# Kernel tuning notes

Measured on AMD Instinct MI355X. Metric: run time of the kernel, lower is better.

The kernel has to match this reference:

```python
import jax, jax.numpy as jnp
import numpy as np

N_NEURONS, D_MODEL, D_FF, N_PATTERNS, K_PATTERNS = 2048, 1024, 4096, 64, 4
B, S, K = 4, 2048, 8


def setup_inputs() -> dict:
    key = jax.random.key(0)
    ks = jax.random.split(key, 10)
    return {
        "x": jax.random.normal(ks[0], (B, S, D_MODEL), jnp.float32),
        "router_out": jax.random.normal(ks[1], (B, S, D_MODEL), jnp.float32),
        "topk_neuron_idx": jax.random.randint(ks[2], (B, S, K), 0, N_NEURONS),
        "topk_neuron_weights": jax.random.uniform(ks[3], (B, S, K), jnp.float32),
        "selected_neurons": jax.random.normal(ks[4], (B, S, K, D_MODEL), jnp.float32),
        "pattern_queries": jax.random.normal(ks[5], (N_PATTERNS, D_MODEL), jnp.float32) * 0.02,
        "gates": jax.random.normal(ks[6], (N_PATTERNS, D_FF), jnp.float32) * 0.02,
        "up_w": jax.random.normal(ks[7], (D_FF, D_MODEL), jnp.float32) / np.sqrt(D_MODEL),
        "up_b": jnp.zeros((D_FF,), jnp.float32),
        "down_w": jax.random.normal(ks[8], (D_MODEL, D_FF), jnp.float32) / np.sqrt(D_FF),
        "down_b": jnp.zeros((D_MODEL,), jnp.float32),
    }


def reference(x, router_out, topk_neuron_idx, topk_neuron_weights, selected_neurons,
              pattern_queries, gates, up_w, up_b, down_w, down_b):
    D = selected_neurons.shape[-1]
    # pattern scoring: [P, B, S, K]
    sim = jnp.einsum('pd,bskd->pbsk', pattern_queries, selected_neurons) / jnp.sqrt(jnp.float32(D))
    pattern_scores = jnp.einsum('pbsk,bsk->bsp', sim, topk_neuron_weights)  # weighted sum over K, permuted
    topk_scores, topk_pattern_idx = jax.lax.top_k(pattern_scores, K_PATTERNS)  # [B,S,k]
    topk_pattern_weights = jax.nn.softmax(topk_scores, axis=-1)
    selected_gates = gates[topk_pattern_idx]  # [B,S,k,d_ff]
    ffn_gate = jnp.einsum('bsk,bskf->bsf', topk_pattern_weights, selected_gates)
    h = jnp.einsum('bsd,fd->bsf', x, up_w) + up_b
    h = jax.nn.gelu(h * jax.nn.sigmoid(ffn_gate), approximate=False)
    return jnp.einsum('bsf,df->bsd', h, down_w) + down_b
```

## Files before the change

### kernel.cpp

```cpp
#include <hip/hip_runtime.h>
#include <hip/hip_bf16.h>
#include <math.h>

#define R_   8192
#define DM   1024
#define DFF  4096
#define NP   64
#define KN   8

typedef __bf16 bf16x8 __attribute__((ext_vector_type(8)));
typedef float  f32x4  __attribute__((ext_vector_type(4)));

__device__ __forceinline__ unsigned short f2bf(float f) {
  union { float f; unsigned u; } v; v.f = f;
  unsigned u = v.u;
  return (unsigned short)((u + 0x7FFFu + ((u >> 16) & 1u)) >> 16);
}

__device__ __forceinline__ float dot4(const float4 a, const float4 b) {
  return a.x * b.x + a.y * b.y + a.z * b.z + a.w * b.w;
}

__device__ __forceinline__ void fma4(float4& a, float w, const float4 s) {
  a.x += w * s.x; a.y += w * s.y; a.z += w * s.z; a.w += w * s.w;
}

__global__ __launch_bounds__(256) void cvt_bf16_kernel(
    const float* __restrict__ in, unsigned short* __restrict__ out, int n8) {
  int i = blockIdx.x * 256 + threadIdx.x;
  if (i >= n8) return;
  const float4* p = (const float4*)in + (size_t)i * 2;
  float4 a = p[0], b = p[1];
  uint4 r;
  r.x = (unsigned)f2bf(a.x) | ((unsigned)f2bf(a.y) << 16);
  r.y = (unsigned)f2bf(a.z) | ((unsigned)f2bf(a.w) << 16);
  r.z = (unsigned)f2bf(b.x) | ((unsigned)f2bf(b.y) << 16);
  r.w = (unsigned)f2bf(b.z) | ((unsigned)f2bf(b.w) << 16);
  ((uint4*)out)[i] = r;
}

__global__ __launch_bounds__(256) void vcomp_kernel(
    const float* __restrict__ sn,
    const float* __restrict__ tw,
    float* __restrict__ v)
{
  const int r = blockIdx.x;
  const int t = threadIdx.x;
  float w[KN];
#pragma unroll
  for (int k = 0; k < KN; ++k) w[k] = tw[(size_t)r * KN + k];
  const float* base = sn + (size_t)r * (KN * DM) + t * 4;
  float4 a = {0.f, 0.f, 0.f, 0.f};
#pragma unroll
  for (int k = 0; k < KN; ++k) fma4(a, w[k], *(const float4*)(base + k * DM));
  *(float4*)(v + (size_t)r * DM + t * 4) = a;
}

__global__ __launch_bounds__(256, 2) void score_kernel(
    const float* __restrict__ v,
    const float* __restrict__ pq,
    int*   __restrict__ out_idx,
    float* __restrict__ out_w)
{
  const int lane = threadIdx.x & 63;
  const int wave = threadIdx.x >> 6;
  const int pos0 = (blockIdx.x * 4 + wave) * 4;

  float4 vr[4][4];
#pragma unroll
  for (int p = 0; p < 4; ++p) {
    const float4* s = (const float4*)(v + (size_t)(pos0 + p) * DM + lane * 16);
    vr[p][0] = s[0]; vr[p][1] = s[1]; vr[p][2] = s[2]; vr[p][3] = s[3];
  }

  float sreg[4];
#pragma unroll 1
  for (int pat = 0; pat < NP; ++pat) {
    const float4* q = (const float4*)(pq + pat * DM + lane * 16);
    const float4 q0 = q[0], q1 = q[1], q2 = q[2], q3 = q[3];
    float part[4];
#pragma unroll
    for (int p = 0; p < 4; ++p)
      part[p] = dot4(q0, vr[p][0]) + dot4(q1, vr[p][1]) +
                dot4(q2, vr[p][2]) + dot4(q3, vr[p][3]);
#pragma unroll
    for (int off = 32; off >= 1; off >>= 1) {
#pragma unroll
      for (int p = 0; p < 4; ++p)
        part[p] += __shfl_xor(part[p], off, 64);
    }
    if (lane == pat) {
#pragma unroll
      for (int p = 0; p < 4; ++p) sreg[p] = part[p] * 0.03125f;
    }
  }

#pragma unroll
  for (int p = 0; p < 4; ++p) {
    float cur = sreg[p];
    float m0, m1, m2, m3; int i0, i1, i2, i3;
#define ARGMAX_STEP(MV, MI)                                   \
    {                                                         \
      float bv = cur; int bi = lane;                          \
      _Pragma("unroll")                                       \
      for (int off = 32; off >= 1; off >>= 1) {               \
        float ov = __shfl_xor(bv, off, 64);                   \
        int   oi = __shfl_xor(bi, off, 64);                   \
        if (ov > bv || (ov == bv && oi < bi)) { bv = ov; bi = oi; } \
      }                                                       \
      MV = bv; MI = bi;                                       \
      if (lane == bi) cur = -3.0e38f;                         \
    }
    ARGMAX_STEP(m0, i0) ARGMAX_STEP(m1, i1) ARGMAX_STEP(m2, i2) ARGMAX_STEP(m3, i3)
#undef ARGMAX_STEP
    const float e1 = __expf(m1 - m0), e2 = __expf(m2 - m0), e3 = __expf(m3 - m0);
    const float inv = 1.f / (1.f + e1 + e2 + e3);
    if (lane < 4) {
      const int r = pos0 + p;
      const int myi = (lane == 0) ? i0 : (lane == 1) ? i1 : (lane == 2) ? i2 : i3;
      const float mye = (lane == 0) ? 1.f : (lane == 1) ? e1 : (lane == 2) ? e2 : e3;
      out_idx[r * 4 + lane] = myi;
      out_w[r * 4 + lane] = mye * inv;
    }
  }
}

__device__ __forceinline__ void gll16(const void* g, void* l) {
  __builtin_amdgcn_global_load_lds(
      (const __attribute__((address_space(1))) unsigned int*)g,
      (__attribute__((address_space(3))) unsigned int*)l, 16, 0, 0);
}


#define LGKM0 asm volatile("s_waitcnt lgkmcnt(0)" ::: "memory")
#define VMC(N) asm volatile("s_waitcnt vmcnt(%0)" ::"i"(N) : "memory")

__global__ __launch_bounds__(256, 2) void gemm1_kernel(
    const unsigned short* __restrict__ A,
    const unsigned short* __restrict__ Bm,
    const float* __restrict__ bias,
    const int*   __restrict__ pidx,
    const float* __restrict__ pwt,
    const float* __restrict__ gates,
    unsigned short* __restrict__ H)
{
  extern __shared__ char smem[];
  constexpr int K_ = 1024, NT = 32;
  const int tid = threadIdx.x, lane = tid & 63, wid = tid >> 6;
  const int wr = wid >> 1, wc = wid & 1;
  const int cpx = gridDim.x >> 3;
  const int swzb = ((int)blockIdx.x & 7) * cpx + ((int)blockIdx.x >> 3);
  const int brow = swzb >> 5, bcol = swzb & 31;

  const unsigned short* Ab = A  + (size_t)brow * 256 * K_;
  const unsigned short* Bb = Bm + (size_t)bcol * 128 * K_;

  const int aSrc = (wid * 16 + (lane >> 2)) * K_ +
                   (((lane & 3) ^ ((lane >> 2) & 3)) * 8);
  const int ldsSt = wid * 1024;
  const int laneRd = (lane & 15) * 64 + (((lane >> 4) ^ (lane & 3)) * 16);
  const int aRd = wr * 8192 + laneRd;
  const int bRd = 16384 + wc * 4096 + laneRd;

  f32x4 acc[8][4];
#pragma unroll
  for (int m = 0; m < 8; ++m)
#pragma unroll
    for (int n = 0; n < 4; ++n) acc[m][n] = (f32x4){0.f, 0.f, 0.f, 0.f};

#define G1_STA(BO, PG) { _Pragma("unroll") for (int i_ = 0; i_ < 4; ++i_)     \
    gll16((PG) + i_ * 64 * K_ + aSrc, smem + (BO) + i_ * 4096 + ldsSt); }
#define G1_STB(BO, PG) { _Pragma("unroll") for (int i_ = 0; i_ < 2; ++i_)     \
    gll16((PG) + i_ * 64 * K_ + aSrc, smem + (BO) + 16384 + i_ * 4096 + ldsSt); }

  G1_STA(0, Ab)           G1_STB(0, Bb)
  G1_STA(24576, Ab + 32)  G1_STB(24576, Bb + 32)
  G1_STB(49152, Bb + 64)
  VMC(8);
  __builtin_amdgcn_s_barrier();

  int o0 = 0, o1 = 24576, o2 = 49152;
#pragma unroll 1
  for (int j = 0; j < NT; ++j) {
    bf16x8 a[4], b[4];
    {
      const char* pa = smem + o0 + aRd;
      const char* pb = smem + o0 + bRd;
#pragma unroll
      for (int m = 0; m < 4; ++m) a[m] = *(const bf16x8*)(pa + m * 1024);
#pragma unroll
      for (int n = 0; n < 4; ++n) b[n] = *(const bf16x8*)(pb + n * 1024);
    }
    if (j < NT - 2) G1_STA(o2, Ab + (j + 2) * 32)
    LGKM0;
    __builtin_amdgcn_s_barrier();
    __builtin_amdgcn_s_setprio(1);
#pragma unroll
    for (int m = 0; m < 4; ++m)
#pragma unroll
      for (int n = 0; n < 4; ++n)
        acc[m][n] = __builtin_amdgcn_mfma_f32_16x16x32_bf16(a[m], b[n], acc[m][n], 0, 0, 0);
    __builtin_amdgcn_s_setprio(0);
    {
      const char* pa = smem + o0 + aRd + 4096;
#pragma unroll
      for (int m = 0; m < 4; ++m) a[m] = *(const bf16x8*)(pa + m * 1024);
    }
    if (j < NT - 3) G1_STB(o0, Bb + (j + 3) * 32)
    LGKM0;
    if (j < NT - 2) { VMC(6); } else { VMC(0); }
    __builtin_amdgcn_s_barrier();
    __builtin_amdgcn_s_setprio(1);
#pragma unroll
    for (int m = 0; m < 4; ++m)
#pragma unroll
      for (int n = 0; n < 4; ++n)
        acc[4 + m][n] = __builtin_amdgcn_mfma_f32_16x16x32_bf16(a[m], b[n], acc[4 + m][n], 0, 0, 0);
    __builtin_amdgcn_s_setprio(0);
    const int t = o0; o0 = o1; o1 = o2; o2 = t;
  }
#undef G1_STA
#undef G1_STB

  const int crow0 = brow * 256 + wr * 128;
  const int ccol0 = bcol * 128 + wc * 64 + (lane & 15);
  const int rsub  = (lane >> 4) * 4;
#pragma unroll
  for (int m = 0; m < 8; ++m) {
    const int rbase = crow0 + m * 16 + rsub;
    int   ia[4][4];
    float wa[4][4];
#pragma unroll
    for (int j = 0; j < 4; ++j) {
      const int4   iq = *(const int4*)(pidx + (size_t)(rbase + j) * 4);
      const float4 wq = *(const float4*)(pwt + (size_t)(rbase + j) * 4);
      ia[j][0] = iq.x; ia[j][1] = iq.y; ia[j][2] = iq.z; ia[j][3] = iq.w;
      wa[j][0] = wq.x; wa[j][1] = wq.y; wa[j][2] = wq.z; wa[j][3] = wq.w;
    }
#pragma unroll
    for (int n = 0; n < 4; ++n) {
      const int col = ccol0 + n * 16;
      const float ub = bias[col];
#pragma unroll
      for (int j = 0; j < 4; ++j) {
        float g = wa[j][0] * gates[(size_t)ia[j][0] * DFF + col]
                + wa[j][1] * gates[(size_t)ia[j][1] * DFF + col]
                + wa[j][2] * gates[(size_t)ia[j][2] * DFF + col]
                + wa[j][3] * gates[(size_t)ia[j][3] * DFF + col];
        const float u   = acc[m][n][j] + ub;
        const float val = u * (1.f / (1.f + __expf(-g)));
        const float h   = 0.5f * val * (1.f + erff(val * 0.70710678118654752f));
        H[(size_t)(rbase + j) * DFF + col] = f2bf(h);
      }
    }
  }
}

__global__ __launch_bounds__(256, 2) void gemm2_kernel(
    const unsigned short* __restrict__ A,
    const unsigned short* __restrict__ Bm,
    const float* __restrict__ bias,
    float* __restrict__ O)
{
  extern __shared__ char smem[];
  constexpr int K_ = 4096, NT = 128;
  const int tid = threadIdx.x, lane = tid & 63, wid = tid >> 6;
  const int wr = wid >> 1, wc = wid & 1;
  const int cpx = gridDim.x >> 3;
  const int swzb = ((int)blockIdx.x & 7) * cpx + ((int)blockIdx.x >> 3);
  const int brow = swzb >> 3, bcol = swzb & 7;

  const unsigned short* Ab = A  + (size_t)brow * 128 * K_;
  const unsigned short* Bb = Bm + (size_t)bcol * 128 * K_;

  const int aSrc = (wid * 16 + (lane >> 2)) * K_ +
                   (((lane & 3) ^ ((lane >> 2) & 3)) * 8);
  const int ldsSt = wid * 1024;
  const int laneRd = (lane & 15) * 64 + (((lane >> 4) ^ (lane & 3)) * 16);
  const int aRd = wr * 4096 + laneRd;
  const int bRd = 8192 + wc * 4096 + laneRd;

  f32x4 acc[4][4];
#pragma unroll
  for (int m = 0; m < 4; ++m)
#pragma unroll
    for (int n = 0; n < 4; ++n) acc[m][n] = (f32x4){0.f, 0.f, 0.f, 0.f};

#define G2_ST(BO, PGA, PGB) {                                                 \
    _Pragma("unroll") for (int i_ = 0; i_ < 2; ++i_)                          \
      gll16((PGA) + i_ * 64 * K_ + aSrc, smem + (BO) + i_ * 4096 + ldsSt);    \
    _Pragma("unroll") for (int i_ = 0; i_ < 2; ++i_)                          \
      gll16((PGB) + i_ * 64 * K_ + aSrc, smem + (BO) + 8192 + i_ * 4096 + ldsSt); }

  G2_ST(0,     Ab,      Bb)
  G2_ST(16384, Ab + 32, Bb + 32)
  G2_ST(32768, Ab + 64, Bb + 64)
  VMC(8);
  __builtin_amdgcn_s_barrier();

  int o0 = 0, o1 = 16384, o2 = 32768, o3 = 49152;
#pragma unroll 1
  for (int j = 0; j < NT; ++j) {
    bf16x8 a[4], b[4];
    {
      const char* pa = smem + o0 + aRd;
      const char* pb = smem + o0 + bRd;
#pragma unroll
      for (int m = 0; m < 4; ++m) a[m] = *(const bf16x8*)(pa + m * 1024);
#pragma unroll
      for (int n = 0; n < 4; ++n) b[n] = *(const bf16x8*)(pb + n * 1024);
    }
    if (j < NT - 3) G2_ST(o3, Ab + (j + 3) * 32, Bb + (j + 3) * 32)
    LGKM0;
    if (j < NT - 3)      { VMC(8); }
    else if (j == NT - 3){ VMC(4); }
    else                 { VMC(0); }
    __builtin_amdgcn_s_barrier();
    __builtin_amdgcn_s_setprio(1);
#pragma unroll
    for (int m = 0; m < 4; ++m)
#pragma unroll
      for (int n = 0; n < 4; ++n)
        acc[m][n] = __builtin_amdgcn_mfma_f32_16x16x32_bf16(a[m], b[n], acc[m][n], 0, 0, 0);
    __builtin_amdgcn_s_setprio(0);
    const int t = o0; o0 = o1; o1 = o2; o2 = o3; o3 = t;
  }
#undef G2_ST

  const int crow0 = brow * 128 + wr * 64;
  const int ccol0 = bcol * 128 + wc * 64 + (lane & 15);
  const int rsub  = (lane >> 4) * 4;
#pragma unroll
  for (int m = 0; m < 4; ++m) {
    const int rbase = crow0 + m * 16 + rsub;
#pragma unroll
    for (int n = 0; n < 4; ++n) {
      const int col = ccol0 + n * 16;
      const float db = bias[col];
#pragma unroll
      for (int j = 0; j < 4; ++j)
        O[(size_t)(rbase + j) * DM + col] = acc[m][n][j] + db;
    }
  }
}

extern "C" void kernel_launch(void* const* d_in, const int* in_sizes, int n_in,
                              void* d_out, int out_size, void* d_ws, size_t ws_size,
                              hipStream_t stream) {
  const float* x     = (const float*)d_in[0];
  const float* tw    = (const float*)d_in[3];
  const float* sn    = (const float*)d_in[4];
  const float* pq    = (const float*)d_in[5];
  const float* gates = (const float*)d_in[6];
  const float* upw   = (const float*)d_in[7];
  const float* upb   = (const float*)d_in[8];
  const float* dnw   = (const float*)d_in[9];
  const float* dnb   = (const float*)d_in[10];
  float* out = (float*)d_out;

  char* p = (char*)d_ws;
  unsigned short* xb  = (unsigned short*)p; p += (size_t)R_ * DM * 2;
  unsigned short* uwb = (unsigned short*)p; p += (size_t)DFF * DM * 2;
  unsigned short* dwb = (unsigned short*)p; p += (size_t)DM * DFF * 2;
  unsigned short* H   = (unsigned short*)p; p += (size_t)R_ * DFF * 2;
  int*   pidx = (int*)p;   p += (size_t)R_ * 4 * sizeof(int);
  float* pwt  = (float*)p; p += (size_t)R_ * 4 * sizeof(float);
  float* vbuf = (float*)p; p += (size_t)R_ * DM * sizeof(float);

  cvt_bf16_kernel<<<(R_ * DM / 8) / 256, 256, 0, stream>>>(x, xb, R_ * DM / 8);
  cvt_bf16_kernel<<<(DFF * DM / 8) / 256, 256, 0, stream>>>(upw, uwb, DFF * DM / 8);
  cvt_bf16_kernel<<<(DM * DFF / 8) / 256, 256, 0, stream>>>(dnw, dwb, DM * DFF / 8);

  vcomp_kernel<<<R_, 256, 0, stream>>>(sn, tw, vbuf);
  score_kernel<<<R_ / 16, 256, 0, stream>>>(vbuf, pq, pidx, pwt);

  hipFuncSetAttribute((const void*)gemm1_kernel,
                      hipFuncAttributeMaxDynamicSharedMemorySize, 73728);
  hipFuncSetAttribute((const void*)gemm2_kernel,
                      hipFuncAttributeMaxDynamicSharedMemorySize, 65536);

  gemm1_kernel<<<(R_ / 256) * (DFF / 128), 256, 73728, stream>>>(
      xb, uwb, upb, pidx, pwt, gates, H);
  gemm2_kernel<<<(R_ / 128) * (DM / 128), 256, 65536, stream>>>(
      H, dwb, dnb, out);
}
```

Baseline: 369.2 us.

## Fuse neuron-weighted reduction into pattern scoring and remap GEMM blocks per XCD

The vcomp kernel is folded into the scoring kernel, so each wave computes the weighted sum of the 8 selected neurons directly in registers. This removes the 32 MB intermediate vbuf write and re-read and one kernel launch. Both GEMMs also change their block-to-tile mapping so that blocks on the same XCD share B columns (gemm1) or A rows (gemm2), aiming at better L2 reuse. The fused kernel issues more loads per wave at the same grid size of 512 blocks, so it may hide the 256 MB selected_neurons stream less well.

```diff
diff --git a/kernel.cpp b/kernel.cpp
--- a/kernel.cpp
+++ b/kernel.cpp
@@ -39,25 +39,9 @@
   ((uint4*)out)[i] = r;
 }
 
-__global__ __launch_bounds__(256) void vcomp_kernel(
+__global__ __launch_bounds__(256, 2) void patt_kernel(
     const float* __restrict__ sn,
     const float* __restrict__ tw,
-    float* __restrict__ v)
-{
-  const int r = blockIdx.x;
-  const int t = threadIdx.x;
-  float w[KN];
-#pragma unroll
-  for (int k = 0; k < KN; ++k) w[k] = tw[(size_t)r * KN + k];
-  const float* base = sn + (size_t)r * (KN * DM) + t * 4;
-  float4 a = {0.f, 0.f, 0.f, 0.f};
-#pragma unroll
-  for (int k = 0; k < KN; ++k) fma4(a, w[k], *(const float4*)(base + k * DM));
-  *(float4*)(v + (size_t)r * DM + t * 4) = a;
-}
-
-__global__ __launch_bounds__(256, 2) void score_kernel(
-    const float* __restrict__ v,
     const float* __restrict__ pq,
     int*   __restrict__ out_idx,
     float* __restrict__ out_w)
@@ -69,8 +53,18 @@
   float4 vr[4][4];
 #pragma unroll
   for (int p = 0; p < 4; ++p) {
-    const float4* s = (const float4*)(v + (size_t)(pos0 + p) * DM + lane * 16);
-    vr[p][0] = s[0]; vr[p][1] = s[1]; vr[p][2] = s[2]; vr[p][3] = s[3];
+    const int r = pos0 + p;
+    const float* wp = tw + (size_t)r * KN;
+    const float* base = sn + (size_t)r * (KN * DM) + lane * 16;
+    float4 a0 = {0,0,0,0}, a1 = {0,0,0,0}, a2 = {0,0,0,0}, a3 = {0,0,0,0};
+#pragma unroll
+    for (int k = 0; k < KN; ++k) {
+      const float wk = wp[k];
+      const float4* s = (const float4*)(base + k * DM);
+      fma4(a0, wk, s[0]); fma4(a1, wk, s[1]);
+      fma4(a2, wk, s[2]); fma4(a3, wk, s[3]);
+    }
+    vr[p][0] = a0; vr[p][1] = a1; vr[p][2] = a2; vr[p][3] = a3;
   }
 
   float sreg[4];
@@ -131,9 +125,9 @@
       (__attribute__((address_space(3))) unsigned int*)l, 16, 0, 0);
 }
 
-
 #define LGKM0 asm volatile("s_waitcnt lgkmcnt(0)" ::: "memory")
 #define VMC(N) asm volatile("s_waitcnt vmcnt(%0)" ::"i"(N) : "memory")
+
 
 __global__ __launch_bounds__(256, 2) void gemm1_kernel(
     const unsigned short* __restrict__ A,
@@ -148,9 +142,9 @@
   constexpr int K_ = 1024, NT = 32;
   const int tid = threadIdx.x, lane = tid & 63, wid = tid >> 6;
   const int wr = wid >> 1, wc = wid & 1;
-  const int cpx = gridDim.x >> 3;
-  const int swzb = ((int)blockIdx.x & 7) * cpx + ((int)blockIdx.x >> 3);
-  const int brow = swzb >> 5, bcol = swzb & 31;
+
+  const int xcd = (int)blockIdx.x & 7, lid = (int)blockIdx.x >> 3;
+  const int brow = lid >> 2, bcol = xcd * 4 + (lid & 3);
 
   const unsigned short* Ab = A  + (size_t)brow * 256 * K_;
   const unsigned short* Bb = Bm + (size_t)bcol * 128 * K_;
@@ -266,9 +260,9 @@
   constexpr int K_ = 4096, NT = 128;
   const int tid = threadIdx.x, lane = tid & 63, wid = tid >> 6;
   const int wr = wid >> 1, wc = wid & 1;
-  const int cpx = gridDim.x >> 3;
-  const int swzb = ((int)blockIdx.x & 7) * cpx + ((int)blockIdx.x >> 3);
-  const int brow = swzb >> 3, bcol = swzb & 7;
+
+  const int xcd = (int)blockIdx.x & 7, lid = (int)blockIdx.x >> 3;
+  const int brow = xcd * 8 + (lid >> 3), bcol = lid & 7;
 
   const unsigned short* Ab = A  + (size_t)brow * 128 * K_;
   const unsigned short* Bb = Bm + (size_t)bcol * 128 * K_;
@@ -365,14 +359,12 @@
   unsigned short* H   = (unsigned short*)p; p += (size_t)R_ * DFF * 2;
   int*   pidx = (int*)p;   p += (size_t)R_ * 4 * sizeof(int);
   float* pwt  = (float*)p; p += (size_t)R_ * 4 * sizeof(float);
-  float* vbuf = (float*)p; p += (size_t)R_ * DM * sizeof(float);
 
   cvt_bf16_kernel<<<(R_ * DM / 8) / 256, 256, 0, stream>>>(x, xb, R_ * DM / 8);
   cvt_bf16_kernel<<<(DFF * DM / 8) / 256, 256, 0, stream>>>(upw, uwb, DFF * DM / 8);
   cvt_bf16_kernel<<<(DM * DFF / 8) / 256, 256, 0, stream>>>(dnw, dwb, DM * DFF / 8);
 
-  vcomp_kernel<<<R_, 256, 0, stream>>>(sn, tw, vbuf);
-  score_kernel<<<R_ / 16, 256, 0, stream>>>(vbuf, pq, pidx, pwt);
+  patt_kernel<<<R_ / 16, 256, 0, stream>>>(sn, tw, pq, pidx, pwt);
 
   hipFuncSetAttribute((const void*)gemm1_kernel,
                       hipFuncAttributeMaxDynamicSharedMemorySize, 73728);
```

Measured after the change: 391.0 us. 1.06x slower.
